# Kernel optimization log

Hardware: AMD Instinct MI355X
Metric: run time of the kernel (lower is better)

## Reference

```python
import jax, jax.numpy as jnp
import numpy as np

V, E, H, C, T = 100000, 300, 512, 40, 4096  # vocab, embed, hidden, num_classes, seq_len


def setup_inputs() -> dict:
    key = jax.random.key(0)
    ks = jax.random.split(key, 19)
    s = lambda k, shape: jax.random.normal(k, shape, jnp.float32) * 0.05
    inp = {"x": jax.random.randint(ks[0], (T,), 0, V, dtype=jnp.int32)}
    inp["emb"] = s(ks[1], (V, E))  # frozen embedding table
    # PyTorch LSTM params, gate order (i, f, g, o); layer0 in=E, layer1 in=2H
    inp["Wih0f"] = s(ks[2], (4 * H, E)); inp["Whh0f"] = s(ks[3], (4 * H, H)); inp["b0f"] = s(ks[4], (4 * H,))
    inp["Wih0b"] = s(ks[5], (4 * H, E)); inp["Whh0b"] = s(ks[6], (4 * H, H)); inp["b0b"] = s(ks[7], (4 * H,))
    inp["Wih1f"] = s(ks[8], (4 * H, 2 * H)); inp["Whh1f"] = s(ks[9], (4 * H, H)); inp["b1f"] = s(ks[10], (4 * H,))
    inp["Wih1b"] = s(ks[11], (4 * H, 2 * H)); inp["Whh1b"] = s(ks[12], (4 * H, H)); inp["b1b"] = s(ks[13], (4 * H,))
    inp["Wc"] = s(ks[14], (C, 2 * H)); inp["bc"] = s(ks[15], (C,))
    inp["trans"] = s(ks[16], (C, C))  # CRF transitions prev->next
    inp["start"] = s(ks[17], (C,)); inp["end"] = s(ks[18], (C,))
    return inp


def _lstm_dir(x, Wih, Whh, b, reverse):
    # x: (T, D) unbatched; returns hidden states (T, H)
    Hd = Whh.shape[1]
    def step(carry, xt):
        h, c = carry
        g = xt @ Wih.T + h @ Whh.T + b  # (4H,)
        i, f, gg, o = jnp.split(g, 4)
        i = jax.nn.sigmoid(i); f = jax.nn.sigmoid(f)
        gg = jnp.tanh(gg); o = jax.nn.sigmoid(o)
        c = f * c + i * gg
        h = o * jnp.tanh(c)
        return (h, c), h
    xs = x[::-1] if reverse else x
    init = (jnp.zeros((Hd,), x.dtype), jnp.zeros((Hd,), x.dtype))
    _, hs = jax.lax.scan(step, init, xs)
    return hs[::-1] if reverse else hs


def _viterbi(emissions, trans, start, end):
    # emissions: (T, C); returns best path (T,) int32
    def fwd(score, em):
        m = score[:, None] + trans  # (C_prev, C_next)
        bp = jnp.argmax(m, axis=0).astype(jnp.int32)
        return jnp.max(m, axis=0) + em, bp
    score0 = start + emissions[0]
    final, bps = jax.lax.scan(fwd, score0, emissions[1:])  # bps: (T-1, C)
    last = jnp.argmax(final + end).astype(jnp.int32)
    def back(tag, bp):
        prev = bp[tag]
        return prev, prev
    _, path = jax.lax.scan(back, last, bps, reverse=True)  # tags 0..T-2 in order
    return jnp.concatenate([path, last[None]])


def reference(x, emb, Wih0f, Whh0f, b0f, Wih0b, Whh0b, b0b, Wih1f, Whh1f, b1f, Wih1b, Whh1b, b1b, Wc, bc, trans, start, end):
    e = emb[x]  # (T, E); dropout is identity at eval
    h0 = jnp.concatenate([_lstm_dir(e, Wih0f, Whh0f, b0f, False),
                          _lstm_dir(e, Wih0b, Whh0b, b0b, True)], axis=-1)  # (T, 2H)
    h1 = jnp.concatenate([_lstm_dir(h0, Wih1f, Whh1f, b1f, False),
                          _lstm_dir(h0, Wih1b, Whh1b, b1b, True)], axis=-1)  # (T, 2H)
    o = h1 @ Wc.T + bc  # (T, C)
    tag_scores = jax.nn.log_softmax(o, axis=1)
    tags = _viterbi(tag_scores, trans, start, end)
    return tag_scores, tags
```

## Files before the change

### kernel.cpp

```cpp
#include <hip/hip_runtime.h>


typedef unsigned int u32;
typedef unsigned long long u64;
typedef u32 u32x4 __attribute__((ext_vector_type(4)));

#define TT 4096
#define HH 512
#define CC 40
#define NG 2048

__device__ __forceinline__ float sigm(float x) { return 1.0f / (1.0f + __expf(-x)); }
__device__ __forceinline__ float tanh_(float x) { return 1.0f - 2.0f / (__expf(2.0f * x) + 1.0f); }

__device__ __forceinline__ void st_agent_u32(u32* p, u32 v) {
    __hip_atomic_store(p, v, __ATOMIC_RELAXED, __HIP_MEMORY_SCOPE_AGENT);
}

__device__ __forceinline__ void ld_mall_b256(const float* p, u32x4& r0, u32x4& r1) {
    asm volatile(
        "global_load_dwordx4 %0, %2, off sc0 sc1\n\t"
        "global_load_dwordx4 %1, %2, off offset:16 sc0 sc1\n\t"
        "s_waitcnt vmcnt(0)"
        : "=&v"(r0), "=&v"(r1)
        : "v"(p)
        : "memory");
}

__global__ __launch_bounds__(256, 2) void gemm_f32_k(const float* __restrict__ A0,
                                                     const float* __restrict__ A1,
                                                     const int* __restrict__ xidx,
                                                     const float* __restrict__ W,
                                                     const float* __restrict__ bias,
                                                     float* __restrict__ C,
                                                     int M, int N, int K, int Ksplit) {
    __shared__ float sA[8][132];
    __shared__ float sW[8][132];
    int tid = threadIdx.x;
    int bn = blockIdx.x, bm = blockIdx.y;
    int tx = tid & 15, ty = tid >> 4;
    int srow = tid >> 1, skh = (tid & 1) * 4;

    int am = bm * 128 + srow;
    const float* arow0;
    const float* arow1 = nullptr;
    if (xidx) {
        arow0 = A0 + (size_t)xidx[am] * K;
    } else {
        arow0 = A0 + (size_t)am * Ksplit;
        arow1 = A1 + (size_t)am * Ksplit;
    }
    const float* wrow = W + (size_t)(bn * 128 + srow) * K;

    float acc[2][2][4][4] = {};

    for (int kc = 0; kc < K; kc += 8) {
        float4 av, wv;
        int k0 = kc + skh;
        if (kc + 8 <= K) {
            if (xidx || k0 + 4 <= Ksplit) av = *(const float4*)(arow0 + k0);
            else                          av = *(const float4*)(arow1 + (k0 - Ksplit));
            wv = *(const float4*)(wrow + k0);
        } else {
            float a_[4], w_[4];
#pragma unroll
            for (int j = 0; j < 4; j++) {
                int k = k0 + j;
                bool ok = k < K;
                a_[j] = ok ? ((xidx || k < Ksplit) ? arow0[k] : arow1[k - Ksplit]) : 0.f;
                w_[j] = ok ? wrow[k] : 0.f;
            }
            av = make_float4(a_[0], a_[1], a_[2], a_[3]);
            wv = make_float4(w_[0], w_[1], w_[2], w_[3]);
        }
        __syncthreads();
        sA[skh + 0][srow] = av.x; sA[skh + 1][srow] = av.y;
        sA[skh + 2][srow] = av.z; sA[skh + 3][srow] = av.w;
        sW[skh + 0][srow] = wv.x; sW[skh + 1][srow] = wv.y;
        sW[skh + 2][srow] = wv.z; sW[skh + 3][srow] = wv.w;
        __syncthreads();
#pragma unroll
        for (int k = 0; k < 8; k++) {
            float4 a0 = *(const float4*)&sA[k][ty * 4];
            float4 a1 = *(const float4*)&sA[k][64 + ty * 4];
            float4 w0 = *(const float4*)&sW[k][tx * 4];
            float4 w1 = *(const float4*)&sW[k][64 + tx * 4];
            float am_[2][4] = {{a0.x, a0.y, a0.z, a0.w}, {a1.x, a1.y, a1.z, a1.w}};
            float wn_[2][4] = {{w0.x, w0.y, w0.z, w0.w}, {w1.x, w1.y, w1.z, w1.w}};
#pragma unroll
            for (int p = 0; p < 2; p++)
#pragma unroll
                for (int q = 0; q < 2; q++)
#pragma unroll
                    for (int mi = 0; mi < 4; mi++)
#pragma unroll
                        for (int ni = 0; ni < 4; ni++)
                            acc[p][q][mi][ni] += am_[p][mi] * wn_[q][ni];
        }
    }

#pragma unroll
    for (int q = 0; q < 2; q++) {
        int gn = bn * 128 + q * 64 + tx * 4;
        float4 b4 = *(const float4*)&bias[gn];
#pragma unroll
        for (int p = 0; p < 2; p++) {
            int gm = bm * 128 + p * 64 + ty * 4;
#pragma unroll
            for (int mi = 0; mi < 4; mi++) {
                float4 o;
                o.x = acc[p][q][mi][0] + b4.x; o.y = acc[p][q][mi][1] + b4.y;
                o.z = acc[p][q][mi][2] + b4.z; o.w = acc[p][q][mi][3] + b4.w;
                *(float4*)&C[(size_t)(gm + mi) * N + gn] = o;
            }
        }
    }
}

__global__ __attribute__((amdgpu_flat_work_group_size(512, 512), amdgpu_waves_per_eu(2, 2)))
void lstm_phase_k(const float* __restrict__ WxF,
                  const float* __restrict__ WxB,
                  const float* __restrict__ WhhF,
                  const float* __restrict__ WhhB,
                  float* __restrict__ histF,
                  float* __restrict__ histB,
                  int phase) {
    const int wg = blockIdx.x & 31;
    const int dir = blockIdx.x >> 5;
    const int tid = threadIdx.x;
    const float* Wx = dir ? WxB : WxF;
    const float* Whh = dir ? WhhB : WhhF;
    float* hist = dir ? histB : histF;
    const u32 ENC = phase ? 0x7F800000u : 0u;

    const int r = tid >> 3, seg = tid & 7;
    const int grow = (r >> 4) * 512 + wg * 16 + (r & 15);

    float w[64];
    {
        const float* wr = Whh + (size_t)grow * HH + seg * 64;
#pragma unroll
        for (int i = 0; i < 16; i++) {
            float4 v = *(const float4*)(wr + i * 4);
            w[i * 4 + 0] = v.x; w[i * 4 + 1] = v.y; w[i * 4 + 2] = v.z; w[i * 4 + 3] = v.w;
        }
    }

    const int j = (tid < 62) ? (tid + (tid >= wg * 2 ? 2 : 0)) : 0;

    __shared__ float lds_h[8 * 68];
    __shared__ float lds_g[64];
    float c_state = 0.f;
    int capped = 0;

    for (int s = 0; s < TT; ++s) {
        const int t = dir ? (TT - 1 - s) : s;
        float wxv = 0.f;
        if (seg == 0) wxv = Wx[(size_t)t * NG + grow];

        if (s > 0) {
            const int tprev = dir ? (t + 1) : (t - 1);
            if (tid < 62) {
                const float* p = hist + (size_t)tprev * HH + j * 8;
                u32x4 v0, v1;
                if (!capped) {
                    int it = 0;
                    for (;;) {
                        ld_mall_b256(p, v0, v1);
                        bool ok;
                        if (phase) {
                            ok = ((v0.x & 0x7F800000u) >= 0x40000000u) &&
                                 ((v0.y & 0x7F800000u) >= 0x40000000u) &&
                                 ((v0.z & 0x7F800000u) >= 0x40000000u) &&
                                 ((v0.w & 0x7F800000u) >= 0x40000000u) &&
                                 ((v1.x & 0x7F800000u) >= 0x40000000u) &&
                                 ((v1.y & 0x7F800000u) >= 0x40000000u) &&
                                 ((v1.z & 0x7F800000u) >= 0x40000000u) &&
                                 ((v1.w & 0x7F800000u) >= 0x40000000u);
                        } else {
                            ok = (v0.x != 0xAAAAAAAAu) && (v0.y != 0xAAAAAAAAu) &&
                                 (v0.z != 0xAAAAAAAAu) && (v0.w != 0xAAAAAAAAu) &&
                                 (v1.x != 0xAAAAAAAAu) && (v1.y != 0xAAAAAAAAu) &&
                                 (v1.z != 0xAAAAAAAAu) && (v1.w != 0xAAAAAAAAu);
                        }
                        if (ok) break;
                        if (++it > (1 << 18)) { capped = 1; break; }
                    }
                } else {
                    ld_mall_b256(p, v0, v1);
                }
                float* dst = &lds_h[(j >> 3) * 68 + ((j & 7) * 8)];
                float4 f0, f1;
                f0.x = __uint_as_float(v0.x ^ ENC); f0.y = __uint_as_float(v0.y ^ ENC);
                f0.z = __uint_as_float(v0.z ^ ENC); f0.w = __uint_as_float(v0.w ^ ENC);
                f1.x = __uint_as_float(v1.x ^ ENC); f1.y = __uint_as_float(v1.y ^ ENC);
                f1.z = __uint_as_float(v1.z ^ ENC); f1.w = __uint_as_float(v1.w ^ ENC);
                *(float4*)dst = f0;
                *(float4*)(dst + 4) = f1;
            }
            __syncthreads();
            float a0 = 0.f, a1 = 0.f, a2 = 0.f, a3 = 0.f;
            const float4* hv4 = (const float4*)&lds_h[seg * 68];
#pragma unroll
            for (int i = 0; i < 16; i++) {
                float4 hv = hv4[i];
                a0 += w[i * 4 + 0] * hv.x;
                a1 += w[i * 4 + 1] * hv.y;
                a2 += w[i * 4 + 2] * hv.z;
                a3 += w[i * 4 + 3] * hv.w;
            }
            float acc = (a0 + a1) + (a2 + a3);
            acc += __shfl_xor(acc, 1);
            acc += __shfl_xor(acc, 2);
            acc += __shfl_xor(acc, 4);
            if (seg == 0) lds_g[r] = acc + wxv;
        } else {
            if (seg == 0) lds_g[r] = wxv;
        }
        __syncthreads();

        if (tid < 16) {
            float gi = lds_g[tid], gf = lds_g[16 + tid], gg = lds_g[32 + tid], go = lds_g[48 + tid];
            float iv = sigm(gi), fv = sigm(gf), gv = tanh_(gg), ov = sigm(go);
            c_state = fv * c_state + iv * gv;
            float h = ov * tanh_(c_state);
            int hidx = wg * 16 + tid;
            lds_h[(hidx >> 6) * 68 + (hidx & 63)] = h;
            st_agent_u32((u32*)&hist[(size_t)t * HH + hidx], __float_as_uint(h) ^ ENC);
        }
    }
}

__global__ __launch_bounds__(64, 4) void classifier_k(const float* __restrict__ histF,
                                                      const float* __restrict__ histB,
                                                      const float* __restrict__ Wc,
                                                      const float* __restrict__ bc,
                                                      float* __restrict__ outsc) {
    int t = blockIdx.x, lane = threadIdx.x;
    __shared__ float hrow[1024];
    const uint4* hf4 = (const uint4*)(histF + (size_t)t * HH);
    const uint4* hb4 = (const uint4*)(histB + (size_t)t * HH);
#pragma unroll
    for (int jj = 0; jj < 4; jj++) {
        int idx4 = jj * 64 + lane;
        uint4 u = (idx4 < 128) ? hf4[idx4] : hb4[idx4 - 128];
        u.x ^= 0x7F800000u; u.y ^= 0x7F800000u; u.z ^= 0x7F800000u; u.w ^= 0x7F800000u;
        float4 v;
        v.x = __uint_as_float(u.x); v.y = __uint_as_float(u.y);
        v.z = __uint_as_float(u.z); v.w = __uint_as_float(u.w);
        *(float4*)&hrow[idx4 * 4] = v;
    }
    __syncthreads();
    float o = 0.f;
    if (lane < CC) {
        o = bc[lane];
        const float4* wr = (const float4*)(Wc + (size_t)lane * 1024);
#pragma unroll 4
        for (int kk = 0; kk < 256; ++kk) {
            float4 w4 = wr[kk];
            float4 h4 = *(const float4*)&hrow[kk * 4];
            o += w4.x * h4.x + w4.y * h4.y + w4.z * h4.z + w4.w * h4.w;
        }
    }
    float m = (lane < CC) ? o : -1e30f;
#pragma unroll
    for (int d = 1; d < 64; d <<= 1) m = fmaxf(m, __shfl_xor(m, d));
    float ex = (lane < CC) ? __expf(o - m) : 0.f;
#pragma unroll
    for (int d = 1; d < 64; d <<= 1) ex += __shfl_xor(ex, d);
    float lse = m + __logf(ex);
    if (lane < CC) outsc[(size_t)t * CC + lane] = o - lse;
}

__global__ __launch_bounds__(64) void viterbi_k(const float* __restrict__ em,
                                               const float* __restrict__ trans,
                                               const float* __restrict__ startv,
                                               const float* __restrict__ endv,
                                               unsigned char* __restrict__ bp,
                                               float* __restrict__ outtags) {
    int lane = threadIdx.x;
    float tcol[CC];
#pragma unroll
    for (int p = 0; p < CC; p++) tcol[p] = 0.f;
    if (lane < CC) {
#pragma unroll
        for (int p = 0; p < CC; p++) tcol[p] = trans[p * CC + lane];
    }
    float s = (lane < CC) ? (startv[lane] + em[lane]) : 0.f;

    for (int t = 1; t < TT; ++t) {
        float emv = (lane < CC) ? em[(size_t)t * CC + lane] : 0.f;
        float b0 = -1e30f, b1 = -1e30f;
        int i0 = 0, i1 = 20;
#pragma unroll
        for (int p = 0; p < 20; p++) {
            float c0 = __shfl(s, p) + tcol[p];
            float c1 = __shfl(s, p + 20) + tcol[p + 20];
            if (c0 > b0) { b0 = c0; i0 = p; }
            if (c1 > b1) { b1 = c1; i1 = p + 20; }
        }
        float best = b0; int bi = i0;
        if (b1 > b0) { best = b1; bi = i1; }
        s = best + emv;
        if (lane < CC) bp[(size_t)t * CC + lane] = (unsigned char)bi;
    }
    float fv = (lane < CC) ? (s + endv[lane]) : -1e30f;
    int fi = (lane < CC) ? lane : 63;
#pragma unroll
    for (int d = 1; d < 64; d <<= 1) {
        float ov = __shfl_xor(fv, d);
        int oi = __shfl_xor(fi, d);
        if (ov > fv || (ov == fv && oi < fi)) { fv = ov; fi = oi; }
    }
    __threadfence();
    if (lane == 0) {
        int cur = fi;
        outtags[TT - 1] = (float)cur;
        for (int t = TT - 2; t >= 0; --t) {
            cur = bp[(size_t)(t + 1) * CC + cur];
            outtags[t] = (float)cur;
        }
    }
}

extern "C" void kernel_launch(void* const* d_in, const int* in_sizes, int n_in,
                              void* d_out, int out_size, void* d_ws, size_t ws_size,
                              hipStream_t stream) {
    const int*   x     = (const int*)d_in[0];
    const float* emb   = (const float*)d_in[1];
    const float* Wih0f = (const float*)d_in[2];
    const float* Whh0f = (const float*)d_in[3];
    const float* b0f   = (const float*)d_in[4];
    const float* Wih0b = (const float*)d_in[5];
    const float* Whh0b = (const float*)d_in[6];
    const float* b0b   = (const float*)d_in[7];
    const float* Wih1f = (const float*)d_in[8];
    const float* Whh1f = (const float*)d_in[9];
    const float* b1f   = (const float*)d_in[10];
    const float* Wih1b = (const float*)d_in[11];
    const float* Whh1b = (const float*)d_in[12];
    const float* b1b   = (const float*)d_in[13];
    const float* Wc    = (const float*)d_in[14];
    const float* bc    = (const float*)d_in[15];
    const float* trans = (const float*)d_in[16];
    const float* startv= (const float*)d_in[17];
    const float* endv  = (const float*)d_in[18];

    char* ws = (char*)d_ws;
    unsigned char* bp = (unsigned char*)(ws + 1024);
    float* WxF  = (float*)(ws + 262144);
    float* WxB  = (float*)(ws + 33816576);
    float* histF= (float*)(ws + 67371008);
    float* histB= (float*)(ws + 75759616);

    if (ws_size < (size_t)84148224) return;

    float* out_sc   = (float*)d_out;
    float* out_tags = out_sc + (size_t)TT * CC;

    gemm_f32_k<<<dim3(16, 32), 256, 0, stream>>>(emb, nullptr, x, Wih0f, b0f, WxF, TT, NG, 300, 300);
    gemm_f32_k<<<dim3(16, 32), 256, 0, stream>>>(emb, nullptr, x, Wih0b, b0b, WxB, TT, NG, 300, 300);
    lstm_phase_k<<<64, 512, 0, stream>>>(WxF, WxB, Whh0f, Whh0b, histF, histB, 0);
    gemm_f32_k<<<dim3(16, 32), 256, 0, stream>>>(histF, histB, nullptr, Wih1f, b1f, WxF, TT, NG, 1024, 512);
    gemm_f32_k<<<dim3(16, 32), 256, 0, stream>>>(histF, histB, nullptr, Wih1b, b1b, WxB, TT, NG, 1024, 512);
    lstm_phase_k<<<64, 512, 0, stream>>>(WxF, WxB, Whh1f, Whh1b, histF, histB, 1);
    classifier_k<<<TT, 64, 0, stream>>>(histF, histB, Wc, bc, out_sc);
    viterbi_k<<<1, 64, 0, stream>>>(out_sc, trans, startv, endv, bp, out_tags);
}
```

Measured before the change: 17.68 ms.

## Make each wave compute its own hidden units, dropping block barriers per step

The recurrent LSTM step is reorganised so each 64-lane wave owns two hidden units with all four gates. Each wave polls and loads the full previous hidden vector from global memory into its own LDS slice, reduces the gate dot products with shuffles, and applies the cell update in registers. This removes both __syncthreads and the shared gate buffer from the per-timestep critical path. In exchange, global polling traffic is eight times higher, since every wave now polls all 512 values, including those produced by its own block.

```diff
diff --git a/kernel.cpp b/kernel.cpp
--- a/kernel.cpp
+++ b/kernel.cpp
@@ -128,13 +128,18 @@
     const int wg = blockIdx.x & 31;
     const int dir = blockIdx.x >> 5;
     const int tid = threadIdx.x;
+    const int wid = tid >> 6;
+    const int lane = tid & 63;
+    const int hsub = lane >> 5;
+    const int gate = (lane >> 3) & 3;
+    const int seg = lane & 7;
     const float* Wx = dir ? WxB : WxF;
     const float* Whh = dir ? WhhB : WhhF;
     float* hist = dir ? histB : histF;
     const u32 ENC = phase ? 0x7F800000u : 0u;
 
-    const int r = tid >> 3, seg = tid & 7;
-    const int grow = (r >> 4) * 512 + wg * 16 + (r & 15);
+    const int hidx = wg * 16 + wid * 2 + hsub;
+    const int grow = gate * 512 + hidx;
 
     float w[64];
     {
@@ -146,10 +151,10 @@
         }
     }
 
-    const int j = (tid < 62) ? (tid + (tid >= wg * 2 ? 2 : 0)) : 0;
-
-    __shared__ float lds_h[8 * 68];
-    __shared__ float lds_g[64];
+    __shared__ float lds_h[8][8 * 68];
+    float* myl = &lds_h[wid][0];
+    float* dst = myl + (lane >> 3) * 68 + (lane & 7) * 8;
+
     float c_state = 0.f;
     int capped = 0;
 
@@ -158,49 +163,46 @@
         float wxv = 0.f;
         if (seg == 0) wxv = Wx[(size_t)t * NG + grow];
 
+        float dot = 0.f;
         if (s > 0) {
             const int tprev = dir ? (t + 1) : (t - 1);
-            if (tid < 62) {
-                const float* p = hist + (size_t)tprev * HH + j * 8;
-                u32x4 v0, v1;
-                if (!capped) {
-                    int it = 0;
-                    for (;;) {
-                        ld_mall_b256(p, v0, v1);
-                        bool ok;
-                        if (phase) {
-                            ok = ((v0.x & 0x7F800000u) >= 0x40000000u) &&
-                                 ((v0.y & 0x7F800000u) >= 0x40000000u) &&
-                                 ((v0.z & 0x7F800000u) >= 0x40000000u) &&
-                                 ((v0.w & 0x7F800000u) >= 0x40000000u) &&
-                                 ((v1.x & 0x7F800000u) >= 0x40000000u) &&
-                                 ((v1.y & 0x7F800000u) >= 0x40000000u) &&
-                                 ((v1.z & 0x7F800000u) >= 0x40000000u) &&
-                                 ((v1.w & 0x7F800000u) >= 0x40000000u);
-                        } else {
-                            ok = (v0.x != 0xAAAAAAAAu) && (v0.y != 0xAAAAAAAAu) &&
-                                 (v0.z != 0xAAAAAAAAu) && (v0.w != 0xAAAAAAAAu) &&
-                                 (v1.x != 0xAAAAAAAAu) && (v1.y != 0xAAAAAAAAu) &&
-                                 (v1.z != 0xAAAAAAAAu) && (v1.w != 0xAAAAAAAAu);
-                        }
-                        if (ok) break;
-                        if (++it > (1 << 18)) { capped = 1; break; }
+            const float* p = hist + (size_t)tprev * HH + lane * 8;
+            u32x4 v0, v1;
+            if (!capped) {
+                int it = 0;
+                for (;;) {
+                    ld_mall_b256(p, v0, v1);
+                    bool ok;
+                    if (phase) {
+                        ok = ((v0.x & 0x7F800000u) >= 0x40000000u) &&
+                             ((v0.y & 0x7F800000u) >= 0x40000000u) &&
+                             ((v0.z & 0x7F800000u) >= 0x40000000u) &&
+                             ((v0.w & 0x7F800000u) >= 0x40000000u) &&
+                             ((v1.x & 0x7F800000u) >= 0x40000000u) &&
+                             ((v1.y & 0x7F800000u) >= 0x40000000u) &&
+                             ((v1.z & 0x7F800000u) >= 0x40000000u) &&
+                             ((v1.w & 0x7F800000u) >= 0x40000000u);
+                    } else {
+                        ok = (v0.x != 0xAAAAAAAAu) && (v0.y != 0xAAAAAAAAu) &&
+                             (v0.z != 0xAAAAAAAAu) && (v0.w != 0xAAAAAAAAu) &&
+                             (v1.x != 0xAAAAAAAAu) && (v1.y != 0xAAAAAAAAu) &&
+                             (v1.z != 0xAAAAAAAAu) && (v1.w != 0xAAAAAAAAu);
                     }
-                } else {
-                    ld_mall_b256(p, v0, v1);
+                    if (ok) break;
+                    if (++it > (1 << 18)) { capped = 1; break; }
                 }
-                float* dst = &lds_h[(j >> 3) * 68 + ((j & 7) * 8)];
-                float4 f0, f1;
-                f0.x = __uint_as_float(v0.x ^ ENC); f0.y = __uint_as_float(v0.y ^ ENC);
-                f0.z = __uint_as_float(v0.z ^ ENC); f0.w = __uint_as_float(v0.w ^ ENC);
-                f1.x = __uint_as_float(v1.x ^ ENC); f1.y = __uint_as_float(v1.y ^ ENC);
-                f1.z = __uint_as_float(v1.z ^ ENC); f1.w = __uint_as_float(v1.w ^ ENC);
-                *(float4*)dst = f0;
-                *(float4*)(dst + 4) = f1;
+            } else {
+                ld_mall_b256(p, v0, v1);
             }
-            __syncthreads();
+            float4 f0, f1;
+            f0.x = __uint_as_float(v0.x ^ ENC); f0.y = __uint_as_float(v0.y ^ ENC);
+            f0.z = __uint_as_float(v0.z ^ ENC); f0.w = __uint_as_float(v0.w ^ ENC);
+            f1.x = __uint_as_float(v1.x ^ ENC); f1.y = __uint_as_float(v1.y ^ ENC);
+            f1.z = __uint_as_float(v1.z ^ ENC); f1.w = __uint_as_float(v1.w ^ ENC);
+            *(float4*)dst = f0;
+            *(float4*)(dst + 4) = f1;
             float a0 = 0.f, a1 = 0.f, a2 = 0.f, a3 = 0.f;
-            const float4* hv4 = (const float4*)&lds_h[seg * 68];
+            const float4* hv4 = (const float4*)(myl + seg * 68);
 #pragma unroll
             for (int i = 0; i < 16; i++) {
                 float4 hv = hv4[i];
@@ -209,25 +211,23 @@
                 a2 += w[i * 4 + 2] * hv.z;
                 a3 += w[i * 4 + 3] * hv.w;
             }
-            float acc = (a0 + a1) + (a2 + a3);
-            acc += __shfl_xor(acc, 1);
-            acc += __shfl_xor(acc, 2);
-            acc += __shfl_xor(acc, 4);
-            if (seg == 0) lds_g[r] = acc + wxv;
-        } else {
-            if (seg == 0) lds_g[r] = wxv;
-        }
-        __syncthreads();
-
-        if (tid < 16) {
-            float gi = lds_g[tid], gf = lds_g[16 + tid], gg = lds_g[32 + tid], go = lds_g[48 + tid];
-            float iv = sigm(gi), fv = sigm(gf), gv = tanh_(gg), ov = sigm(go);
-            c_state = fv * c_state + iv * gv;
-            float h = ov * tanh_(c_state);
-            int hidx = wg * 16 + tid;
-            lds_h[(hidx >> 6) * 68 + (hidx & 63)] = h;
+            dot = (a0 + a1) + (a2 + a3);
+        }
+
+        float acc = dot + wxv;
+        acc += __shfl_xor(acc, 1);
+        acc += __shfl_xor(acc, 2);
+        acc += __shfl_xor(acc, 4);
+        const int base = (lane & 32) + seg;
+        float gi = __shfl(acc, base + 0);
+        float gf = __shfl(acc, base + 8);
+        float gg = __shfl(acc, base + 16);
+        float go = __shfl(acc, base + 24);
+        float iv = sigm(gi), fv = sigm(gf), gv = tanh_(gg), ov = sigm(go);
+        c_state = fv * c_state + iv * gv;
+        float h = ov * tanh_(c_state);
+        if ((lane & 31) == 0)
             st_agent_u32((u32*)&hist[(size_t)t * HH + hidx], __float_as_uint(h) ^ ENC);
-        }
     }
 }
 
```

After: 36.47 ms. +106.3%, slower.
